# Kernel tuning notes

Measured on AMD Instinct MI355X. Metric: run time of the kernel, lower is better.

The kernel has to match this reference:

```python
import jax, jax.numpy as jnp
import numpy as np

H = 512
TEMPERATURE = 1.0


def setup_inputs() -> dict:
    key = jax.random.key(0)
    ks = jax.random.split(key, 9)
    B, Q, S = 4, 64, 1024
    scale = 1.0 / np.sqrt(H)
    return {
        "query": jax.random.normal(ks[0], (B, Q, H), jnp.float32),
        "key_": jax.random.normal(ks[1], (B, S, H), jnp.float32),
        "value": jax.random.normal(ks[2], (B, S, H), jnp.float32),
        "Wq": jax.random.normal(ks[3], (H, H), jnp.float32) * scale,
        "bq": jax.random.normal(ks[4], (H,), jnp.float32) * 0.01,
        "Wk": jax.random.normal(ks[5], (H, H), jnp.float32) * scale,
        "bk": jax.random.normal(ks[6], (H,), jnp.float32) * 0.01,
        "we": jax.random.normal(ks[7], (H,), jnp.float32) * scale,
        "be": jax.random.normal(ks[8], (), jnp.float32) * 0.01,
    }


def reference(query, key_, value, Wq, bq, Wk, bk, we, be):
    # query: [B,Q,H], key_/value: [B,S,H]
    qp = jnp.einsum("bqd,dh->bqh", query, Wq) + bq          # [B,Q,H]
    kp = jnp.einsum("bsd,dh->bsh", key_, Wk) + bk           # [B,S,H]
    attn_sum = jnp.tanh(qp[:, :, None, :] + kp[:, None, :, :])  # [B,Q,S,H]
    scores = (jnp.einsum("bqsh,h->bqs", attn_sum, we) + be) / TEMPERATURE
    weights = jax.nn.softmax(scores, axis=-1)               # [B,Q,S]
    context = jnp.einsum("bqs,bsh->bqh", weights, value)    # [B,Q,H]
    return context, weights
```

## Files before the change

### kernel.cpp

```cpp
#include <hip/hip_runtime.h>


constexpr int kB = 4;
constexpr int kQ = 64;
constexpr int kS = 1024;
constexpr int kH = 512;

typedef short bf16x8 __attribute__((ext_vector_type(8)));
typedef float f32x4 __attribute__((ext_vector_type(4)));

__device__ __forceinline__ unsigned bf16rtn_bits(float x) {
  unsigned u = __float_as_uint(x);
  u += 0x7FFFu + ((u >> 16) & 1u);
  return u;
}

__device__ __forceinline__ void glds16(const void* g, void* l) {
  __builtin_amdgcn_global_load_lds(
      (__attribute__((address_space(1))) void*)(g),
      (__attribute__((address_space(3))) void*)(l), 16, 0, 0);
}

__global__ __launch_bounds__(256) void convert_all(
    const float* __restrict__ Wk, const float* __restrict__ Wq,
    const float* __restrict__ key_, const float* __restrict__ query,
    const float* __restrict__ we,
    unsigned short* __restrict__ Bhi, unsigned short* __restrict__ Blo,
    unsigned short* __restrict__ Xhi, unsigned short* __restrict__ Xlo,
    float* __restrict__ wsum4) {
  __shared__ __align__(16) unsigned short LHi[128 * 40];
  __shared__ __align__(16) unsigned short LLo[128 * 40];
  const int bid = blockIdx.x;
  const int t = threadIdx.x;
  if (bid == 800) {
    const int w = t >> 6, ln = t & 63;
    float v = we[w * 128 + ln] + we[w * 128 + 64 + ln];
#pragma unroll
    for (int off = 32; off; off >>= 1) v += __shfl_xor(v, off);
    if (ln == 0) wsum4[w] = v;
    return;
  }
  if (bid < 256) {
    const int gid = bid * 256 + t;
    const int c = gid & 63;
    const int g = (gid >> 6) & 3;
    const int kt = (gid >> 8) & 15;
    const int ct = (gid >> 12) & 7;
    const int mat = gid >> 15;
    const float* W = mat ? Wq : Wk;
    const float* src = W + (size_t)(kt * 32 + g * 8) * kH + ct * 64 + c;
    bf16x8 hv, lv;
#pragma unroll
    for (int j = 0; j < 8; j++) {
      float x = src[(size_t)j * kH];
      unsigned u = bf16rtn_bits(x);
      float hf = __uint_as_float(u & 0xFFFF0000u);
      unsigned v = bf16rtn_bits(x - hf);
      hv[j] = (short)(u >> 16);
      lv[j] = (short)(v >> 16);
    }
    *(bf16x8*)(Bhi + (size_t)gid * 8) = hv;
    *(bf16x8*)(Blo + (size_t)gid * 8) = lv;
    return;
  }
  const int xb = bid - 256;
  const int kt = xb & 15;
  const int rt = xb >> 4;
  const float* X = (rt < 32) ? (key_ + (size_t)rt * 128 * kH)
                             : (query + (size_t)(rt - 32) * 128 * kH);
  const int r = t >> 1, c0 = (t & 1) * 16;
  const float* src = X + (size_t)r * kH + kt * 32 + c0;
  bf16x8 hv0, hv1, lv0, lv1;
#pragma unroll
  for (int i = 0; i < 16; i++) {
    float x = src[i];
    unsigned u = bf16rtn_bits(x);
    float hf = __uint_as_float(u & 0xFFFF0000u);
    unsigned v = bf16rtn_bits(x - hf);
    if (i < 8) { hv0[i] = (short)(u >> 16); lv0[i] = (short)(v >> 16); }
    else       { hv1[i - 8] = (short)(u >> 16); lv1[i - 8] = (short)(v >> 16); }
  }
  *(bf16x8*)&LHi[r * 40 + c0] = hv0;
  *(bf16x8*)&LHi[r * 40 + c0 + 8] = hv1;
  *(bf16x8*)&LLo[r * 40 + c0] = lv0;
  *(bf16x8*)&LLo[r * 40 + c0 + 8] = lv1;
  __syncthreads();
  const size_t obase = (size_t)(rt * 16 + kt) * 512 * 8;
#pragma unroll
  for (int p = 0; p < 2; p++) {
    const int s = t + p * 256;
    const int rr = s & 127, g = s >> 7;
    *(uint4*)(Xhi + obase + (size_t)s * 8) = *(const uint4*)&LHi[rr * 40 + g * 8];
    *(uint4*)(Xlo + obase + (size_t)s * 8) = *(const uint4*)&LLo[rr * 40 + g * 8];
  }
}

__global__ __launch_bounds__(256) void proj_mfma(
    const unsigned short* __restrict__ Xhi, const unsigned short* __restrict__ Xlo,
    const unsigned short* __restrict__ Bhi, const unsigned short* __restrict__ Blo,
    const float* __restrict__ bk, const float* __restrict__ bq,
    float* __restrict__ EkT, float* __restrict__ Eq) {
  __shared__ __align__(16) unsigned short SMEM[3 * 8192];

  const int bid = blockIdx.y * 8 + blockIdx.x;
  int ct, rt;
  if (bid < 512) {
    ct = (bid >> 3) & 7;
    rt = (bid & 7) + 8 * (bid >> 6);
  } else {
    const int tb = bid - 512;
    ct = tb >> 2;
    rt = 64 + (tb & 3);
  }

  const int mat = (rt >= 64) ? 1 : 0;
  const float* bias = mat ? bq : bk;

  const int t = threadIdx.x;
  const int rt128 = rt >> 1, hhalf = rt & 1;
  const int ga_slot = ((t >> 6) << 7) + (hhalf << 6) + (t & 63);
  const unsigned short* gah = Xhi + ((size_t)(rt128 * 16) * 512 + ga_slot) * 8;
  const unsigned short* gal = Xlo + ((size_t)(rt128 * 16) * 512 + ga_slot) * 8;
  const unsigned short* gbh = Bhi + (((size_t)(mat * 8 + ct) * 16) * 256 + t) * 8;
  const unsigned short* gbl = Blo + (((size_t)(mat * 8 + ct) * 16) * 256 + t) * 8;

  auto stage = [&](int buf, int kt2) {
    unsigned short* base = SMEM + buf * 8192;
    glds16(gah + (size_t)kt2 * 512 * 8, base + t * 8);
    glds16(gal + (size_t)kt2 * 512 * 8, base + 2048 + t * 8);
    glds16(gbh + (size_t)kt2 * 256 * 8, base + 4096 + t * 8);
    glds16(gbl + (size_t)kt2 * 256 * 8, base + 6144 + t * 8);
  };

  const int l = t & 63, lg = l >> 4, lr = l & 15;
  const int wv = t >> 6, wm = wv >> 1, wn = wv & 1;
  const int oa0 = (lg * 64 + wm * 32 + lr) * 8;
  const int ob0 = (lg * 64 + wn * 32 + lr) * 8;

  f32x4 acc[2][2];
#pragma unroll
  for (int m = 0; m < 2; m++)
#pragma unroll
    for (int n = 0; n < 2; n++) acc[m][n] = {0.f, 0.f, 0.f, 0.f};

  stage(0, 0);
  stage(1, 1);

#pragma unroll
  for (int kt2 = 0; kt2 < 16; kt2++) {
    if (kt2 < 15) asm volatile("s_waitcnt vmcnt(4)" ::: "memory");
    else          asm volatile("s_waitcnt vmcnt(0)" ::: "memory");
    __builtin_amdgcn_s_barrier();
    __builtin_amdgcn_sched_barrier(0);

    const unsigned short* base = SMEM + (kt2 % 3) * 8192;
    bf16x8 ah[2], al[2], bh[2], bl[2];
#pragma unroll
    for (int m = 0; m < 2; m++) {
      ah[m] = *(const bf16x8*)(base + oa0 + m * 128);
      al[m] = *(const bf16x8*)(base + 2048 + oa0 + m * 128);
    }
#pragma unroll
    for (int n = 0; n < 2; n++) {
      bh[n] = *(const bf16x8*)(base + 4096 + ob0 + n * 128);
      bl[n] = *(const bf16x8*)(base + 6144 + ob0 + n * 128);
    }
    if (kt2 < 14) stage((kt2 + 2) % 3, kt2 + 2);
#pragma unroll
    for (int m = 0; m < 2; m++)
#pragma unroll
      for (int n = 0; n < 2; n++) {
        acc[m][n] = __builtin_amdgcn_mfma_f32_16x16x32_bf16(ah[m], bh[n], acc[m][n], 0, 0, 0);
        acc[m][n] = __builtin_amdgcn_mfma_f32_16x16x32_bf16(al[m], bh[n], acc[m][n], 0, 0, 0);
        acc[m][n] = __builtin_amdgcn_mfma_f32_16x16x32_bf16(ah[m], bl[n], acc[m][n], 0, 0, 0);
      }
    __builtin_amdgcn_sched_barrier(0);
  }

  const int colL = wn * 32 + lr;
  const int col0 = ct * 64 + colL;
  const float b0 = bias[col0];
  const float b1 = bias[col0 + 16];

  if (mat == 0) {
    __syncthreads();
    float (*T)[65] = (float(*)[65])SMEM;
#pragma unroll
    for (int m = 0; m < 2; m++) {
      const int row0 = wm * 32 + m * 16 + lg * 4;
#pragma unroll
      for (int jj = 0; jj < 4; jj++) {
        T[row0 + jj][colL]      = __expf(2.f * (acc[m][0][jj] + b0));
        T[row0 + jj][colL + 16] = __expf(2.f * (acc[m][1][jj] + b1));
      }
    }
    __syncthreads();
    const int sl = t & 63;
    const int cb = (t >> 6) * 16;
    const int R = rt * 64 + sl;
    const int bb = R >> 10, ss = R & 1023;
    float* outp = EkT + ((size_t)(bb * kH + ct * 64)) * kS + ss;
#pragma unroll
    for (int i = 0; i < 16; i++)
      outp[(size_t)(cb + i) * kS] = T[sl][cb + i];
  } else {
    float* Y = Eq + (size_t)(rt - 64) * 64 * kH;
#pragma unroll
    for (int m = 0; m < 2; m++) {
      const int row0 = wm * 32 + m * 16 + lg * 4;
#pragma unroll
      for (int jj = 0; jj < 4; jj++) {
        float* y = Y + (size_t)(row0 + jj) * kH;
        y[col0]      = __expf(2.f * (acc[m][0][jj] + b0));
        y[col0 + 16] = __expf(2.f * (acc[m][1][jj] + b1));
      }
    }
  }
}

__global__ __launch_bounds__(256) void score_kernel(
    const float* __restrict__ Eq, const float* __restrict__ EkT,
    const float* __restrict__ wsum4, const float* __restrict__ we,
    float* __restrict__ sraw4) {
  const int t = threadIdx.x, lane = t & 63;
  const int wvu = __builtin_amdgcn_readfirstlane(t >> 6);
  const int u = blockIdx.x * 4 + wvu;
  const int hq = u & 3, st = (u >> 2) & 15, qp = (u >> 6) & 31, b = u >> 11;
  const int s = st * 64 + lane;
  const int q0g = b * kQ + qp * 2;
  const int h0 = hq * 128;

  const float4* w4 = (const float4*)(we + h0);
  const float4* qa4 = (const float4*)(Eq + (size_t)q0g * kH + h0);
  const float4* qb4 = (const float4*)(Eq + (size_t)(q0g + 1) * kH + h0);
  const float* ek = EkT + ((size_t)(b * kH + h0)) * kS + s;
  const float wsum = wsum4[hq];

  float accA = 0.f, accB = 0.f;
#pragma unroll 4
  for (int g = 0; g < 32; g++) {
    const float4 w = w4[g];
    const float4 qa = qa4[g];
    const float4 qb = qb4[g];
    const float e0 = ek[(size_t)(4 * g + 0) * kS];
    const float e1 = ek[(size_t)(4 * g + 1) * kS];
    const float e2 = ek[(size_t)(4 * g + 2) * kS];
    const float e3 = ek[(size_t)(4 * g + 3) * kS];
    {
      float a1 = fmaf(qa.x, e0, 1.f), c1 = fmaf(qa.y, e1, 1.f);
      accA = fmaf(fmaf(w.y, a1, w.x * c1), __builtin_amdgcn_rcpf(a1 * c1), accA);
      float a2 = fmaf(qa.z, e2, 1.f), c2 = fmaf(qa.w, e3, 1.f);
      accA = fmaf(fmaf(w.w, a2, w.z * c2), __builtin_amdgcn_rcpf(a2 * c2), accA);
    }
    {
      float a1 = fmaf(qb.x, e0, 1.f), c1 = fmaf(qb.y, e1, 1.f);
      accB = fmaf(fmaf(w.y, a1, w.x * c1), __builtin_amdgcn_rcpf(a1 * c1), accB);
      float a2 = fmaf(qb.z, e2, 1.f), c2 = fmaf(qb.w, e3, 1.f);
      accB = fmaf(fmaf(w.w, a2, w.z * c2), __builtin_amdgcn_rcpf(a2 * c2), accB);
    }
  }

  float* plane = sraw4 + (size_t)hq * kB * kQ * kS;
  plane[(size_t)(q0g + 0) * kS + s] = fmaf(-2.f, accA, wsum);
  plane[(size_t)(q0g + 1) * kS + s] = fmaf(-2.f, accB, wsum);
}

__global__ __launch_bounds__(256) void ctx_fused(
    const float* __restrict__ sraw4, const float* __restrict__ value,
    float* __restrict__ wout, float* __restrict__ ctx) {
  __shared__ __align__(16) float wt[4][1024];
  __shared__ __align__(16) float parts[4][4][128];
  const int bid = blockIdx.x;
  const int qc = bid >> 4, b = (bid >> 2) & 3, hc = bid & 3;
  const int t = threadIdx.x, wv = t >> 6, lane = t & 63;
  const int grow = b * kQ + qc * 4 + wv;

  const size_t plane = (size_t)kB * kQ * kS / 4;
  const float4* r0 = (const float4*)(sraw4) + (size_t)grow * (kS / 4);
  const float4* r1 = r0 + plane;
  const float4* r2 = r1 + plane;
  const float4* r3 = r2 + plane;
  float4 v[4];
#pragma unroll
  for (int j = 0; j < 4; j++) {
    const int idx = lane + 64 * j;
    float4 p0 = r0[idx], p1 = r1[idx], p2 = r2[idx], p3 = r3[idx];
    v[j].x = (p0.x + p1.x) + (p2.x + p3.x);
    v[j].y = (p0.y + p1.y) + (p2.y + p3.y);
    v[j].z = (p0.z + p1.z) + (p2.z + p3.z);
    v[j].w = (p0.w + p1.w) + (p2.w + p3.w);
  }
  float m = -1e30f;
#pragma unroll
  for (int j = 0; j < 4; j++)
    m = fmaxf(m, fmaxf(fmaxf(v[j].x, v[j].y), fmaxf(v[j].z, v[j].w)));
#pragma unroll
  for (int off = 32; off; off >>= 1) m = fmaxf(m, __shfl_xor(m, off));
  float sum = 0.f;
#pragma unroll
  for (int j = 0; j < 4; j++) {
    v[j].x = __expf(v[j].x - m); v[j].y = __expf(v[j].y - m);
    v[j].z = __expf(v[j].z - m); v[j].w = __expf(v[j].w - m);
    sum += v[j].x + v[j].y + v[j].z + v[j].w;
  }
#pragma unroll
  for (int off = 32; off; off >>= 1) sum += __shfl_xor(sum, off);
  const float inv = 1.f / sum;
  float4* wrow = (float4*)&wt[wv][0];
  float4* gw = (float4*)(wout + (size_t)grow * kS);
#pragma unroll
  for (int j = 0; j < 4; j++) {
    v[j].x *= inv; v[j].y *= inv; v[j].z *= inv; v[j].w *= inv;
    wrow[lane + 64 * j] = v[j];
    if (hc == 0) gw[lane + 64 * j] = v[j];
  }
  __syncthreads();

  const float* vbase =
      value + ((size_t)b * kS + wv * 256) * kH + hc * 128 + lane * 2;
  float2 acc[4];
#pragma unroll
  for (int q = 0; q < 4; q++) acc[q] = {0.f, 0.f};
#pragma unroll 2
  for (int s4 = 0; s4 < 64; s4++) {
    float4 wq[4];
#pragma unroll
    for (int q = 0; q < 4; q++)
      wq[q] = *(const float4*)&wt[q][wv * 256 + s4 * 4];
#pragma unroll
    for (int uu = 0; uu < 4; uu++) {
      const float2 vv = *(const float2*)(vbase + (size_t)(s4 * 4 + uu) * kH);
      const float w0 = ((const float*)&wq[0])[uu];
      const float w1 = ((const float*)&wq[1])[uu];
      const float w2 = ((const float*)&wq[2])[uu];
      const float w3 = ((const float*)&wq[3])[uu];
      acc[0].x = fmaf(w0, vv.x, acc[0].x); acc[0].y = fmaf(w0, vv.y, acc[0].y);
      acc[1].x = fmaf(w1, vv.x, acc[1].x); acc[1].y = fmaf(w1, vv.y, acc[1].y);
      acc[2].x = fmaf(w2, vv.x, acc[2].x); acc[2].y = fmaf(w2, vv.y, acc[2].y);
      acc[3].x = fmaf(w3, vv.x, acc[3].x); acc[3].y = fmaf(w3, vv.y, acc[3].y);
    }
  }
#pragma unroll
  for (int q = 0; q < 4; q++)
    *(float2*)&parts[wv][q][lane * 2] = acc[q];
  __syncthreads();

  const int q = t >> 6, hp = t & 63;
  float2 r = {0.f, 0.f};
#pragma unroll
  for (int w = 0; w < 4; w++) {
    const float2 p2 = *(const float2*)&parts[w][q][hp * 2];
    r.x += p2.x; r.y += p2.y;
  }
  *(float2*)(ctx + (size_t)(b * kQ + qc * 4 + q) * kH + hc * 128 + hp * 2) = r;
}

extern "C" void kernel_launch(void* const* d_in, const int* in_sizes, int n_in,
                              void* d_out, int out_size, void* d_ws,
                              size_t ws_size, hipStream_t stream) {
  const float* query = (const float*)d_in[0];
  const float* key_  = (const float*)d_in[1];
  const float* value = (const float*)d_in[2];
  const float* Wq    = (const float*)d_in[3];
  const float* bq    = (const float*)d_in[4];
  const float* Wk    = (const float*)d_in[5];
  const float* bk    = (const float*)d_in[6];
  const float* we    = (const float*)d_in[7];

  float* ctx  = (float*)d_out;
  float* wout = (float*)d_out + (size_t)kB * kQ * kH;

  float* Eq    = (float*)d_ws;
  float* sraw4 = Eq + (size_t)kB * kQ * kH;
  unsigned short* Bhi =
      (unsigned short*)((char*)d_ws + (size_t)(kB * kQ * kH + kB * kS * kH) * 4);
  unsigned short* Blo = Bhi + (size_t)2 * 8 * 16 * 256 * 8;
  unsigned short* Xhi = Blo + (size_t)2 * 8 * 16 * 256 * 8;
  unsigned short* Xlo = Xhi + (size_t)34 * 16 * 512 * 8;
  float* EkT = (float*)(Xlo + (size_t)34 * 16 * 512 * 8);
  float* wsum4 = EkT + (size_t)4 * 512 * 1024;

  convert_all<<<801, 256, 0, stream>>>(Wk, Wq, key_, query, we, Bhi, Blo, Xhi,
                                       Xlo, wsum4);
  proj_mfma<<<dim3(8, 68), 256, 0, stream>>>(Xhi, Xlo, Bhi, Blo, bk, bq, EkT, Eq);
  score_kernel<<<2048, 256, 0, stream>>>(Eq, EkT, wsum4, we, sraw4);
  ctx_fused<<<256, 256, 0, stream>>>(sraw4, value, wout, ctx);
}
```

Before: 134.8 us.

## Interleave EkT in float4 groups and compute four queries per wave

After: 132.5 us. No clear change (-1.7%).

```diff
diff --git a/kernel.cpp b/kernel.cpp
--- a/kernel.cpp
+++ b/kernel.cpp
@@ -99,7 +99,7 @@
     const unsigned short* __restrict__ Xhi, const unsigned short* __restrict__ Xlo,
     const unsigned short* __restrict__ Bhi, const unsigned short* __restrict__ Blo,
     const float* __restrict__ bk, const float* __restrict__ bq,
-    float* __restrict__ EkT, float* __restrict__ Eq) {
+    float* __restrict__ EkT4, float* __restrict__ Eq) {
   __shared__ __align__(16) unsigned short SMEM[3 * 8192];
 
   const int bid = blockIdx.y * 8 + blockIdx.x;
@@ -199,10 +199,14 @@
     const int cb = (t >> 6) * 16;
     const int R = rt * 64 + sl;
     const int bb = R >> 10, ss = R & 1023;
-    float* outp = EkT + ((size_t)(bb * kH + ct * 64)) * kS + ss;
-#pragma unroll
-    for (int i = 0; i < 16; i++)
-      outp[(size_t)(cb + i) * kS] = T[sl][cb + i];
+    float* outp =
+        EkT4 + (((size_t)(bb * 128 + ((ct * 64 + cb) >> 2))) * 1024 + ss) * 4;
+#pragma unroll
+    for (int j = 0; j < 4; j++) {
+      float4 v4 = {T[sl][cb + 4 * j + 0], T[sl][cb + 4 * j + 1],
+                   T[sl][cb + 4 * j + 2], T[sl][cb + 4 * j + 3]};
+      *(float4*)(outp + (size_t)j * 1024 * 4) = v4;
+    }
   } else {
     float* Y = Eq + (size_t)(rt - 64) * 64 * kH;
 #pragma unroll
@@ -219,50 +223,53 @@
 }
 
 __global__ __launch_bounds__(256) void score_kernel(
-    const float* __restrict__ Eq, const float* __restrict__ EkT,
+    const float* __restrict__ Eq, const float* __restrict__ EkT4,
     const float* __restrict__ wsum4, const float* __restrict__ we,
     float* __restrict__ sraw4) {
   const int t = threadIdx.x, lane = t & 63;
   const int wvu = __builtin_amdgcn_readfirstlane(t >> 6);
   const int u = blockIdx.x * 4 + wvu;
-  const int hq = u & 3, st = (u >> 2) & 15, qp = (u >> 6) & 31, b = u >> 11;
+  const int hq = u & 3, st = (u >> 2) & 15, qo = (u >> 6) & 15, b = u >> 10;
   const int s = st * 64 + lane;
-  const int q0g = b * kQ + qp * 2;
+  const int q0g = b * kQ + qo * 4;
   const int h0 = hq * 128;
 
   const float4* w4 = (const float4*)(we + h0);
-  const float4* qa4 = (const float4*)(Eq + (size_t)q0g * kH + h0);
+  const float4* qa4 = (const float4*)(Eq + (size_t)(q0g + 0) * kH + h0);
   const float4* qb4 = (const float4*)(Eq + (size_t)(q0g + 1) * kH + h0);
-  const float* ek = EkT + ((size_t)(b * kH + h0)) * kS + s;
+  const float4* qc4 = (const float4*)(Eq + (size_t)(q0g + 2) * kH + h0);
+  const float4* qd4 = (const float4*)(Eq + (size_t)(q0g + 3) * kH + h0);
+  const float* ek = EkT4 + ((size_t)(b * 128 + (h0 >> 2)) * 1024 + s) * 4;
   const float wsum = wsum4[hq];
 
-  float accA = 0.f, accB = 0.f;
+  float acc0 = 0.f, acc1 = 0.f, acc2 = 0.f, acc3 = 0.f;
 #pragma unroll 4
   for (int g = 0; g < 32; g++) {
+    const float4 e = *(const float4*)(ek + (size_t)g * 4096);
     const float4 w = w4[g];
     const float4 qa = qa4[g];
     const float4 qb = qb4[g];
-    const float e0 = ek[(size_t)(4 * g + 0) * kS];
-    const float e1 = ek[(size_t)(4 * g + 1) * kS];
-    const float e2 = ek[(size_t)(4 * g + 2) * kS];
-    const float e3 = ek[(size_t)(4 * g + 3) * kS];
-    {
-      float a1 = fmaf(qa.x, e0, 1.f), c1 = fmaf(qa.y, e1, 1.f);
-      accA = fmaf(fmaf(w.y, a1, w.x * c1), __builtin_amdgcn_rcpf(a1 * c1), accA);
-      float a2 = fmaf(qa.z, e2, 1.f), c2 = fmaf(qa.w, e3, 1.f);
-      accA = fmaf(fmaf(w.w, a2, w.z * c2), __builtin_amdgcn_rcpf(a2 * c2), accA);
-    }
-    {
-      float a1 = fmaf(qb.x, e0, 1.f), c1 = fmaf(qb.y, e1, 1.f);
-      accB = fmaf(fmaf(w.y, a1, w.x * c1), __builtin_amdgcn_rcpf(a1 * c1), accB);
-      float a2 = fmaf(qb.z, e2, 1.f), c2 = fmaf(qb.w, e3, 1.f);
-      accB = fmaf(fmaf(w.w, a2, w.z * c2), __builtin_amdgcn_rcpf(a2 * c2), accB);
-    }
+    const float4 qc = qc4[g];
+    const float4 qd = qd4[g];
+#define SCORE_PAIR(accv, qv)                                                  \
+  {                                                                           \
+    float a1 = fmaf(qv.x, e.x, 1.f), c1 = fmaf(qv.y, e.y, 1.f);               \
+    accv = fmaf(fmaf(w.y, a1, w.x * c1), __builtin_amdgcn_rcpf(a1 * c1), accv);\
+    float a2 = fmaf(qv.z, e.z, 1.f), c2 = fmaf(qv.w, e.w, 1.f);               \
+    accv = fmaf(fmaf(w.w, a2, w.z * c2), __builtin_amdgcn_rcpf(a2 * c2), accv);\
+  }
+    SCORE_PAIR(acc0, qa)
+    SCORE_PAIR(acc1, qb)
+    SCORE_PAIR(acc2, qc)
+    SCORE_PAIR(acc3, qd)
+#undef SCORE_PAIR
   }
 
   float* plane = sraw4 + (size_t)hq * kB * kQ * kS;
-  plane[(size_t)(q0g + 0) * kS + s] = fmaf(-2.f, accA, wsum);
-  plane[(size_t)(q0g + 1) * kS + s] = fmaf(-2.f, accB, wsum);
+  plane[(size_t)(q0g + 0) * kS + s] = fmaf(-2.f, acc0, wsum);
+  plane[(size_t)(q0g + 1) * kS + s] = fmaf(-2.f, acc1, wsum);
+  plane[(size_t)(q0g + 2) * kS + s] = fmaf(-2.f, acc2, wsum);
+  plane[(size_t)(q0g + 3) * kS + s] = fmaf(-2.f, acc3, wsum);
 }
 
 __global__ __launch_bounds__(256) void ctx_fused(
@@ -377,12 +384,12 @@
   unsigned short* Blo = Bhi + (size_t)2 * 8 * 16 * 256 * 8;
   unsigned short* Xhi = Blo + (size_t)2 * 8 * 16 * 256 * 8;
   unsigned short* Xlo = Xhi + (size_t)34 * 16 * 512 * 8;
-  float* EkT = (float*)(Xlo + (size_t)34 * 16 * 512 * 8);
-  float* wsum4 = EkT + (size_t)4 * 512 * 1024;
+  float* EkT4 = (float*)(Xlo + (size_t)34 * 16 * 512 * 8);
+  float* wsum4 = EkT4 + (size_t)4 * 512 * 1024;
 
   convert_all<<<801, 256, 0, stream>>>(Wk, Wq, key_, query, we, Bhi, Blo, Xhi,
                                        Xlo, wsum4);
-  proj_mfma<<<dim3(8, 68), 256, 0, stream>>>(Xhi, Xlo, Bhi, Blo, bk, bq, EkT, Eq);
-  score_kernel<<<2048, 256, 0, stream>>>(Eq, EkT, wsum4, we, sraw4);
+  proj_mfma<<<dim3(8, 68), 256, 0, stream>>>(Xhi, Xlo, Bhi, Blo, bk, bq, EkT4, Eq);
+  score_kernel<<<1024, 256, 0, stream>>>(Eq, EkT4, wsum4, we, sraw4);
   ctx_fused<<<256, 256, 0, stream>>>(sraw4, value, wout, ctx);
 }
```
